# Kernel tuning notes

Measured on AMD Instinct MI355X. Metric: run time of the kernel, lower is better.

## Reference

```python
import jax, jax.numpy as jnp
import numpy as np

EMB = 1024
HEADS = 16


def setup_inputs() -> dict:
    key = jax.random.key(0)
    ks = jax.random.split(key, 5)
    s = 1.0 / np.sqrt(EMB).astype(np.float32)
    return {
        "x": jax.random.normal(ks[0], (4, 2048, EMB), dtype=jnp.float32),
        "Wq": jax.random.normal(ks[1], (EMB, EMB), dtype=jnp.float32) * s,
        "bq": jnp.zeros((EMB,), dtype=jnp.float32),
        "Wk": jax.random.normal(ks[2], (EMB, EMB), dtype=jnp.float32) * s,
        "bk": jnp.zeros((EMB,), dtype=jnp.float32),
        "Wv": jax.random.normal(ks[3], (EMB, EMB), dtype=jnp.float32) * s,
        "bv": jnp.zeros((EMB,), dtype=jnp.float32),
        "Wo": jax.random.normal(ks[4], (EMB, EMB), dtype=jnp.float32) * s,
        "bo": jnp.zeros((EMB,), dtype=jnp.float32),
    }


def reference(x, Wq, bq, Wk, bk, Wv, bv, Wo, bo):
    b, n, e = x.shape
    h = HEADS
    d = e // h
    # QKV projections, split heads: [b, n, e] -> [b, h, n, d]
    def split_heads(t):
        return t.reshape(b, n, h, d).transpose(0, 2, 1, 3)
    q = split_heads(x @ Wq + bq)
    k = split_heads(x @ Wk + bk)
    v = split_heads(x @ Wv + bv)
    # NOTE: original scales by sqrt(emb_size), not sqrt(head_dim)
    energy = jnp.einsum('bhqd,bhkd->bhqk', q, k)
    att = jax.nn.softmax(energy / jnp.sqrt(jnp.float32(e)), axis=-1)
    # dropout is identity in eval mode
    out = jnp.einsum('bhqk,bhkd->bhqd', att, v)
    out = out.transpose(0, 2, 1, 3).reshape(b, n, e)
    return out @ Wo + bo
```

## Files before the change

### kernel.cpp

```cpp
#include <hip/hip_runtime.h>

#define EMB   1024
#define SEQ   2048
#define BATCH 4
#define HEADS 16
#define HDIM  64
#define MTOT  8192

typedef __bf16 bf16x8 __attribute__((ext_vector_type(8)));
typedef float  fx4    __attribute__((ext_vector_type(4)));

#if __has_builtin(__builtin_amdgcn_exp2f)
#define EXP2(x) __builtin_amdgcn_exp2f(x)
#else
#define EXP2(x) exp2f(x)
#endif

__device__ __forceinline__ unsigned short f2bf(float f) {
    unsigned u = __builtin_bit_cast(unsigned, f);
    u += 0x7fffu + ((u >> 16) & 1u);
    return (unsigned short)(u >> 16);
}
__device__ __forceinline__ unsigned short bfbits(float f) {
    __bf16 h = (__bf16)f;
    return __builtin_bit_cast(unsigned short, h);
}

#define AS1 __attribute__((address_space(1)))
#define AS3 __attribute__((address_space(3)))
__device__ __forceinline__ void glds16(const void* g, void* l) {
    __builtin_amdgcn_global_load_lds((AS1 void*)g, (AS3 void*)l, 16, 0, 0);
}
#define DRAIN_GLDS() __builtin_amdgcn_s_waitcnt(0x0f70)

#define QSCALE 0.0450842137604569f

__global__ __launch_bounds__(256) void cvt_x_kernel(const float* __restrict__ x,
                                                    unsigned short* __restrict__ xb)
{
    const int idx = (blockIdx.x * 256 + threadIdx.x) * 4;
    const float4 v = *(const float4*)(x + idx);
    ushort4 o;
    o.x = f2bf(v.x); o.y = f2bf(v.y); o.z = f2bf(v.z); o.w = f2bf(v.w);
    *(ushort4*)(xb + idx) = o;
}

__global__ __launch_bounds__(256) void cvt_w_kernel(
    const float* __restrict__ w0, const float* __restrict__ w1,
    const float* __restrict__ w2, const float* __restrict__ w3,
    unsigned short* __restrict__ o0, unsigned short* __restrict__ o1,
    unsigned short* __restrict__ o2, unsigned short* __restrict__ o3)
{
    const int z = blockIdx.z;
    const float* W = z == 0 ? w0 : (z == 1 ? w1 : (z == 2 ? w2 : w3));
    unsigned short* O = z == 0 ? o0 : (z == 1 ? o1 : (z == 2 ? o2 : o3));

    __shared__ float Ws[64][65];
    const int t  = threadIdx.x;
    const int k0 = blockIdx.x * 64, n0 = blockIdx.y * 64;
#pragma unroll
    for (int p = 0; p < 4; ++p) {
        const int row = p * 16 + (t >> 4);
        const int col = (t & 15) * 4;
        const float4 v = *(const float4*)(W + (size_t)(k0 + row) * EMB + n0 + col);
        Ws[row][col]     = v.x; Ws[row][col + 1] = v.y;
        Ws[row][col + 2] = v.z; Ws[row][col + 3] = v.w;
    }
    __syncthreads();
    const int nn = t >> 2;
    const int kb = (t & 3) * 16;
#pragma unroll
    for (int q = 0; q < 2; ++q) {
        const int kk = kb + q * 8;
        ushort4 u0, u1;
        u0.x = f2bf(Ws[kk + 0][nn]); u0.y = f2bf(Ws[kk + 1][nn]);
        u0.z = f2bf(Ws[kk + 2][nn]); u0.w = f2bf(Ws[kk + 3][nn]);
        u1.x = f2bf(Ws[kk + 4][nn]); u1.y = f2bf(Ws[kk + 5][nn]);
        u1.z = f2bf(Ws[kk + 6][nn]); u1.w = f2bf(Ws[kk + 7][nn]);
        *(ushort4*)(O + (size_t)(n0 + nn) * EMB + k0 + kk)     = u0;
        *(ushort4*)(O + (size_t)(n0 + nn) * EMB + k0 + kk + 4) = u1;
    }
}

__global__ __launch_bounds__(256) void gemm_bf16_kernel(
    const unsigned short* __restrict__ Ag,
    const unsigned short* __restrict__ B0, const unsigned short* __restrict__ B1,
    const unsigned short* __restrict__ B2,
    const float* __restrict__ bias0, const float* __restrict__ bias1,
    const float* __restrict__ bias2,
    void* out0, void* out1, void* out2, int mode)
{
    const int z = blockIdx.z;
    const unsigned short* __restrict__ Bg = z == 0 ? B0 : (z == 1 ? B1 : B2);
    const float* __restrict__ bias = z == 0 ? bias0 : (z == 1 ? bias1 : bias2);
    void* outp = z == 0 ? out0 : (z == 1 ? out1 : out2);

    __shared__ unsigned short As[128][32];
    __shared__ unsigned short Bs[128][32];

    const int t    = threadIdx.x;
    const int w    = t >> 6;
    const int lane = t & 63;
    const int low4 = lane & 15;
    const int quad = lane >> 4;
    const int m0 = blockIdx.x * 128;
    const int e0 = blockIdx.y * 128;
    const int we = (w & 1) * 64;
    const int wm = (w >> 1) * 64;

    const int srow   = w * 32 + (lane >> 2);
    const int schunk = (lane & 3) ^ ((lane >> 3) & 3);
    const int scol   = schunk * 8;

    const int fchunk = (quad ^ ((low4 >> 1) & 3)) * 8;

    fx4 acc[4][4] = {};

    for (int k0 = 0; k0 < EMB; k0 += 32) {
        __syncthreads();
        glds16(Ag + (size_t)(m0 + srow) * EMB + k0 + scol,      &As[w * 32][0]);
        glds16(Ag + (size_t)(m0 + srow + 16) * EMB + k0 + scol, &As[w * 32 + 16][0]);
        glds16(Bg + (size_t)(e0 + srow) * EMB + k0 + scol,      &Bs[w * 32][0]);
        glds16(Bg + (size_t)(e0 + srow + 16) * EMB + k0 + scol, &Bs[w * 32 + 16][0]);
        DRAIN_GLDS();
        __syncthreads();

        bf16x8 af[4], bfr[4];
#pragma unroll
        for (int i = 0; i < 4; ++i) {
            af[i]  = *(const bf16x8*)&Bs[we + i * 16 + low4][fchunk];
            bfr[i] = *(const bf16x8*)&As[wm + i * 16 + low4][fchunk];
        }
#pragma unroll
        for (int i = 0; i < 4; ++i)
#pragma unroll
            for (int j = 0; j < 4; ++j)
                acc[i][j] = __builtin_amdgcn_mfma_f32_16x16x32_bf16(af[i], bfr[j], acc[i][j], 0, 0, 0);
    }

    fx4 bv[4];
#pragma unroll
    for (int i = 0; i < 4; ++i)
        bv[i] = *(const fx4*)(bias + e0 + we + i * 16 + quad * 4);

    if (mode == 1) {
#pragma unroll
        for (int i = 0; i < 4; ++i)
#pragma unroll
            for (int j = 0; j < 4; ++j) {
                const int m  = m0 + wm + j * 16 + low4;
                const int eb = e0 + we + i * 16 + quad * 4;
                fx4 o4;
#pragma unroll
                for (int rr = 0; rr < 4; ++rr) o4[rr] = acc[i][j][rr] + bv[i][rr];
                *(fx4*)((float*)outp + (size_t)m * EMB + eb) = o4;
            }
    } else if (z <= 1) {
        const float sc = (z == 0) ? QSCALE : 1.0f;
        unsigned short* o = (unsigned short*)outp;
#pragma unroll
        for (int i = 0; i < 4; ++i)
#pragma unroll
            for (int j = 0; j < 4; ++j) {
                const int m  = m0 + wm + j * 16 + low4;
                const int eb = e0 + we + i * 16 + quad * 4;
                const int bb = m >> 11, n = m & (SEQ - 1);
                const int hh = eb >> 6, db = eb & 63;
                ushort4 o4;
                o4.x = f2bf((acc[i][j][0] + bv[i][0]) * sc);
                o4.y = f2bf((acc[i][j][1] + bv[i][1]) * sc);
                o4.z = f2bf((acc[i][j][2] + bv[i][2]) * sc);
                o4.w = f2bf((acc[i][j][3] + bv[i][3]) * sc);
                *(ushort4*)(o + (((size_t)(bb * HEADS + hh)) * SEQ + n) * HDIM + db) = o4;
            }
    } else {
        unsigned short* o = (unsigned short*)outp;
        const int mbase = m0 + wm;
        const int bb    = mbase >> 11;
        const int nb    = mbase & (SEQ - 1);
#pragma unroll
        for (int i = 0; i < 4; ++i) {
            const int eb = e0 + we + i * 16 + quad * 4;
            const int hh = eb >> 6, db = eb & 63;
#pragma unroll
            for (int rr = 0; rr < 4; ++rr) {
                ushort4 o4;
                o4.x = f2bf(acc[i][0][rr] + bv[i][rr]);
                o4.y = f2bf(acc[i][1][rr] + bv[i][rr]);
                o4.z = f2bf(acc[i][2][rr] + bv[i][rr]);
                o4.w = f2bf(acc[i][3][rr] + bv[i][rr]);
                *(ushort4*)(o + (((size_t)(bb * HEADS + hh)) * HDIM + db + rr) * SEQ
                              + nb + low4 * 4) = o4;
            }
        }
    }
}

__global__ __launch_bounds__(256, 2) void attn_mfma5_kernel(
    const unsigned short* __restrict__ qg, const unsigned short* __restrict__ kg,
    const unsigned short* __restrict__ vg, unsigned short* __restrict__ attb)
{
    __shared__ unsigned short Ks[2][64][64];
    __shared__ unsigned short Vs[2][64][64];

    const int t    = threadIdx.x;
    const int w    = t >> 6;
    const int lane = t & 63;
    const int low4 = lane & 15;
    const int quad = lane >> 4;
    const int q0   = blockIdx.x * 256 + w * 64;
    const int bh   = blockIdx.y;
    const size_t base = (size_t)bh * SEQ * HDIM;

    const int srow8  = lane >> 3;
    const int schunk = (lane & 7) ^ srow8;

    const int tr  = 2 * (low4 >> 2) + (low4 & 1) + 8 * ((low4 >> 1) & 1);
    const int x7k = tr & 7;
    const int x7v = low4 & 7;

    bf16x8 aq[4][2];
#pragma unroll
    for (int s = 0; s < 4; ++s) {
        const size_t qrow = base + (size_t)(q0 + s * 16 + low4) * HDIM;
        aq[s][0] = *(const bf16x8*)(qg + qrow + quad * 8);
        aq[s][1] = *(const bf16x8*)(qg + qrow + 32 + quad * 8);
    }

    fx4 o_acc[4][4] = {};
    float l_part[4] = {};
    const fx4 fzero = {0.f, 0.f, 0.f, 0.f};

    {
        const unsigned short* kp = kg + base + (size_t)(w * 16 + srow8) * HDIM + schunk * 8;
        glds16(kp,              &Ks[0][w * 16][0]);
        glds16(kp + 8 * HDIM,   &Ks[0][w * 16 + 8][0]);
        const unsigned short* vp = vg + base + (size_t)(w * 16 + srow8) * SEQ + schunk * 8;
        glds16(vp,              &Vs[0][w * 16][0]);
        glds16(vp + 8 * SEQ,    &Vs[0][w * 16 + 8][0]);
    }

    for (int tt0 = 0; tt0 < SEQ / 64; ++tt0) {
        const int buf = tt0 & 1;
        DRAIN_GLDS();
        __syncthreads();

        bf16x8 kf[4][2], vf[4][2];
#pragma unroll
        for (int tk = 0; tk < 4; ++tk) {
#pragma unroll
            for (int c = 0; c < 2; ++c) {
                kf[tk][c] = *(const bf16x8*)&Ks[buf][tk * 16 + tr][(((c * 4 + quad) ^ x7k)) * 8];
                vf[tk][c] = *(const bf16x8*)&Vs[buf][tk * 16 + low4][(((c * 4 + quad) ^ x7v)) * 8];
            }
        }

        if (tt0 + 1 < SEQ / 64) {
            const int kv1 = (tt0 + 1) * 64;
            const unsigned short* kp = kg + base + (size_t)(kv1 + w * 16 + srow8) * HDIM + schunk * 8;
            glds16(kp,            &Ks[buf ^ 1][w * 16][0]);
            glds16(kp + 8 * HDIM, &Ks[buf ^ 1][w * 16 + 8][0]);
            const unsigned short* vp = vg + base + (size_t)(w * 16 + srow8) * SEQ + kv1 + schunk * 8;
            glds16(vp,            &Vs[buf ^ 1][w * 16][0]);
            glds16(vp + 8 * SEQ,  &Vs[buf ^ 1][w * 16 + 8][0]);
        }

#pragma unroll
        for (int s = 0; s < 4; ++s) {
            fx4 sa[4];
#pragma unroll
            for (int tk = 0; tk < 4; ++tk) {
                sa[tk] = __builtin_amdgcn_mfma_f32_16x16x32_bf16(kf[tk][0], aq[s][0], fzero, 0, 0, 0);
                sa[tk] = __builtin_amdgcn_mfma_f32_16x16x32_bf16(kf[tk][1], aq[s][1], sa[tk], 0, 0, 0);
            }
            float p[4][4];
#pragma unroll
            for (int tk = 0; tk < 4; ++tk)
#pragma unroll
                for (int r = 0; r < 4; ++r)
                    p[tk][r] = EXP2(sa[tk][r]);

            l_part[s] += (((p[0][0] + p[0][1]) + (p[0][2] + p[0][3]))
                        + ((p[1][0] + p[1][1]) + (p[1][2] + p[1][3])))
                       + (((p[2][0] + p[2][1]) + (p[2][2] + p[2][3]))
                        + ((p[3][0] + p[3][1]) + (p[3][2] + p[3][3])));

            bf16x8 pf0, pf1;
#pragma unroll
            for (int tk = 0; tk < 4; ++tk) {
                pf0[tk]     = (__bf16)p[tk][0];
                pf0[4 + tk] = (__bf16)p[tk][1];
                pf1[tk]     = (__bf16)p[tk][2];
                pf1[4 + tk] = (__bf16)p[tk][3];
            }
#pragma unroll
            for (int t2 = 0; t2 < 4; ++t2) {
                o_acc[s][t2] = __builtin_amdgcn_mfma_f32_16x16x32_bf16(vf[t2][0], pf0, o_acc[s][t2], 0, 0, 0);
                o_acc[s][t2] = __builtin_amdgcn_mfma_f32_16x16x32_bf16(vf[t2][1], pf1, o_acc[s][t2], 0, 0, 0);
            }
        }
    }

    float linv[4];
#pragma unroll
    for (int s = 0; s < 4; ++s) {
        float v = l_part[s];
        v += __shfl_xor(v, 16);
        v += __shfl_xor(v, 32);
        linv[s] = 1.0f / v;
    }

    const int bb = bh >> 4, hh = bh & 15;
#pragma unroll
    for (int s = 0; s < 4; ++s) {
        const size_t m = (size_t)bb * SEQ + q0 + s * 16 + low4;
#pragma unroll
        for (int t2 = 0; t2 < 4; ++t2) {
            ushort4 o4;
            o4.x = bfbits(o_acc[s][t2][0] * linv[s]);
            o4.y = bfbits(o_acc[s][t2][1] * linv[s]);
            o4.z = bfbits(o_acc[s][t2][2] * linv[s]);
            o4.w = bfbits(o_acc[s][t2][3] * linv[s]);
            *(ushort4*)(attb + m * EMB + hh * HDIM + t2 * 16 + quad * 4) = o4;
        }
    }
}

extern "C" void kernel_launch(void* const* d_in, const int* in_sizes, int n_in,
                              void* d_out, int out_size, void* d_ws, size_t ws_size,
                              hipStream_t stream)
{
    const float* x  = (const float*)d_in[0];
    const float* Wq = (const float*)d_in[1];
    const float* bq = (const float*)d_in[2];
    const float* Wk = (const float*)d_in[3];
    const float* bk = (const float*)d_in[4];
    const float* Wv = (const float*)d_in[5];
    const float* bv = (const float*)d_in[6];
    const float* Wo = (const float*)d_in[7];
    const float* bo = (const float*)d_in[8];

    unsigned short* ws  = (unsigned short*)d_ws;
    unsigned short* xb  = ws;
    unsigned short* wqt = xb + 8388608;
    unsigned short* wkt = wqt + 1048576;
    unsigned short* wvt = wkt + 1048576;
    unsigned short* wot = wvt + 1048576;
    unsigned short* qb  = wot + 1048576;
    unsigned short* kbuf = qb + 8388608;
    unsigned short* vtb  = kbuf + 8388608;
    unsigned short* attb = vtb + 8388608;

    cvt_x_kernel<<<8192, 256, 0, stream>>>(x, xb);
    cvt_w_kernel<<<dim3(16, 16, 4), 256, 0, stream>>>(Wq, Wk, Wv, Wo, wqt, wkt, wvt, wot);

    gemm_bf16_kernel<<<dim3(64, 8, 3), 256, 0, stream>>>(
        xb, wqt, wkt, wvt, bq, bk, bv, qb, kbuf, vtb, 0);

    attn_mfma5_kernel<<<dim3(8, 64), 256, 0, stream>>>(qb, kbuf, vtb, attb);

    gemm_bf16_kernel<<<dim3(64, 8, 1), 256, 0, stream>>>(
        attb, wot, wot, wot, bo, bo, bo, d_out, d_out, d_out, 1);
}
```

Measured before the change: 271.0 us.

## Replace QKV projection with 256x256-tile double-buffered fused GEMM kernel

Adds a dedicated QKV projection kernel that uses 256x256 output tiles, 512 threads, a 64-wide K step and double-buffered LDS staging through global_load_lds, with a swizzled block order for L2 locality. It treats Wq/Wk/Wv as one contiguous 3072-row weight matrix, which relies on their transposed copies being adjacent in the workspace. The goal is more data reuse per tile and overlap of loads with MFMA compared with the old 128x128 single-buffered GEMM. The cost is high register and LDS pressure (128 KB of LDS per block), which may limit occupancy.

```diff
diff --git a/kernel.cpp b/kernel.cpp
--- a/kernel.cpp
+++ b/kernel.cpp
@@ -32,6 +32,10 @@
     __builtin_amdgcn_global_load_lds((AS1 void*)g, (AS3 void*)l, 16, 0, 0);
 }
 #define DRAIN_GLDS() __builtin_amdgcn_s_waitcnt(0x0f70)
+
+#define BAR()    asm volatile("s_barrier" ::: "memory")
+#define WAITV8() asm volatile("s_waitcnt vmcnt(8)" ::: "memory")
+#define WAITV0() asm volatile("s_waitcnt vmcnt(0)" ::: "memory")
 
 #define QSCALE 0.0450842137604569f
 
@@ -82,6 +86,171 @@
     }
 }
 
+__device__ __forceinline__ void stage8(const unsigned short* xp, unsigned short* xd,
+                                       const unsigned short* wp, unsigned short* wd)
+{
+    glds16(xp,            xd);
+    glds16(xp +  8 * EMB, xd + 8 * 64);
+    glds16(xp + 16 * EMB, xd + 16 * 64);
+    glds16(xp + 24 * EMB, xd + 24 * 64);
+    glds16(wp,            wd);
+    glds16(wp +  8 * EMB, wd + 8 * 64);
+    glds16(wp + 16 * EMB, wd + 16 * 64);
+    glds16(wp + 24 * EMB, wd + 24 * 64);
+}
+
+__global__ __launch_bounds__(512, 2) void gemm_qkv256_kernel(
+    const unsigned short* __restrict__ Xg, const unsigned short* __restrict__ Wg,
+    const float* __restrict__ bq, const float* __restrict__ bk,
+    const float* __restrict__ bv,
+    unsigned short* __restrict__ qb, unsigned short* __restrict__ kb,
+    unsigned short* __restrict__ vtb)
+{
+    __shared__ unsigned short Xs[2][256][64];
+    __shared__ unsigned short Ws[2][256][64];
+
+    int lin = blockIdx.x;
+    lin = (lin & 7) * 48 + (lin >> 3);
+    const int bx  = lin & 31;
+    const int by  = lin >> 5;
+    const int m0  = bx * 256;
+    const int e0g = by * 256;
+
+    const int t    = threadIdx.x;
+    const int w    = t >> 6;
+    const int lane = t & 63;
+    const int low4 = lane & 15;
+    const int quad = lane >> 4;
+    const int wm   = w >> 2;
+    const int wn   = w & 3;
+
+    const int r8 = lane >> 3;
+    const int sc = (lane & 7) ^ r8;
+
+    const unsigned short* xrow = Xg + (size_t)(m0 + w * 32 + r8) * EMB + sc * 8;
+    const unsigned short* wrow = Wg + (size_t)(e0g + w * 32 + r8) * EMB + sc * 8;
+
+    fx4 acc[4][8] = {};
+
+    stage8(xrow,      &Xs[0][w * 32][0], wrow,      &Ws[0][w * 32][0]);
+    stage8(xrow + 64, &Xs[1][w * 32][0], wrow + 64, &Ws[1][w * 32][0]);
+    WAITV8();
+    BAR();
+
+#pragma unroll 2
+    for (int kt = 0; kt < 16; ++kt) {
+        unsigned short (*Xb)[64] = Xs[kt & 1];
+        unsigned short (*Wb)[64] = Ws[kt & 1];
+
+        {
+            bf16x8 wf[4], xf[8];
+#pragma unroll
+            for (int ni = 0; ni < 4; ++ni) {
+                const int row = wn * 64 + ni * 16 + low4;
+                wf[ni] = *(const bf16x8*)&Wb[row][((quad) ^ (row & 7)) * 8];
+            }
+#pragma unroll
+            for (int mi = 0; mi < 8; ++mi) {
+                const int row = wm * 128 + mi * 16 + low4;
+                xf[mi] = *(const bf16x8*)&Xb[row][((quad) ^ (row & 7)) * 8];
+            }
+            BAR();
+            __builtin_amdgcn_s_setprio(1);
+#pragma unroll
+            for (int ni = 0; ni < 4; ++ni)
+#pragma unroll
+                for (int mi = 0; mi < 8; ++mi)
+                    acc[ni][mi] = __builtin_amdgcn_mfma_f32_16x16x32_bf16(
+                        wf[ni], xf[mi], acc[ni][mi], 0, 0, 0);
+            __builtin_amdgcn_s_setprio(0);
+            BAR();
+        }
+        {
+            bf16x8 wf[4], xf[8];
+#pragma unroll
+            for (int ni = 0; ni < 4; ++ni) {
+                const int row = wn * 64 + ni * 16 + low4;
+                wf[ni] = *(const bf16x8*)&Wb[row][((4 + quad) ^ (row & 7)) * 8];
+            }
+#pragma unroll
+            for (int mi = 0; mi < 8; ++mi) {
+                const int row = wm * 128 + mi * 16 + low4;
+                xf[mi] = *(const bf16x8*)&Xb[row][((4 + quad) ^ (row & 7)) * 8];
+            }
+            BAR();
+            __builtin_amdgcn_s_setprio(1);
+#pragma unroll
+            for (int ni = 0; ni < 4; ++ni)
+#pragma unroll
+                for (int mi = 0; mi < 8; ++mi)
+                    acc[ni][mi] = __builtin_amdgcn_mfma_f32_16x16x32_bf16(
+                        wf[ni], xf[mi], acc[ni][mi], 0, 0, 0);
+            __builtin_amdgcn_s_setprio(0);
+            BAR();
+        }
+        if (kt + 2 < 16) {
+            stage8(xrow + (kt + 2) * 64, &Xb[w * 32][0],
+                   wrow + (kt + 2) * 64, &Wb[w * 32][0]);
+            WAITV8();
+            BAR();
+        } else if (kt + 1 < 16) {
+            WAITV0();
+            BAR();
+        }
+    }
+
+    const int z   = by >> 2;
+    const int eLb = (by & 3) * 256 + wn * 64;
+    const float* bias = z == 0 ? bq : (z == 1 ? bk : bv);
+    fx4 bvv[4];
+#pragma unroll
+    for (int ni = 0; ni < 4; ++ni)
+        bvv[ni] = *(const fx4*)(bias + eLb + ni * 16 + quad * 4);
+
+    if (z <= 1) {
+        const float scl = (z == 0) ? QSCALE : 1.0f;
+        unsigned short* o = (z == 0) ? qb : kb;
+#pragma unroll
+        for (int ni = 0; ni < 4; ++ni)
+#pragma unroll
+            for (int mi = 0; mi < 8; ++mi) {
+                const int m  = m0 + wm * 128 + mi * 16 + low4;
+                const int eL = eLb + ni * 16 + quad * 4;
+                const int bb = m >> 11, n = m & (SEQ - 1);
+                const int hh = eL >> 6, db = eL & 63;
+                ushort4 o4;
+                o4.x = f2bf((acc[ni][mi][0] + bvv[ni][0]) * scl);
+                o4.y = f2bf((acc[ni][mi][1] + bvv[ni][1]) * scl);
+                o4.z = f2bf((acc[ni][mi][2] + bvv[ni][2]) * scl);
+                o4.w = f2bf((acc[ni][mi][3] + bvv[ni][3]) * scl);
+                *(ushort4*)(o + (((size_t)(bb * HEADS + hh)) * SEQ + n) * HDIM + db) = o4;
+            }
+    } else {
+        unsigned short* o = vtb;
+#pragma unroll
+        for (int ni = 0; ni < 4; ++ni) {
+            const int eL = eLb + ni * 16 + quad * 4;
+            const int hh = eL >> 6, db = eL & 63;
+#pragma unroll
+            for (int g = 0; g < 2; ++g) {
+                const int mb = m0 + wm * 128 + g * 64;
+                const int bb = mb >> 11;
+                const int nb = mb & (SEQ - 1);
+#pragma unroll
+                for (int rr = 0; rr < 4; ++rr) {
+                    ushort4 o4;
+                    o4.x = f2bf(acc[ni][g * 4 + 0][rr] + bvv[ni][rr]);
+                    o4.y = f2bf(acc[ni][g * 4 + 1][rr] + bvv[ni][rr]);
+                    o4.z = f2bf(acc[ni][g * 4 + 2][rr] + bvv[ni][rr]);
+                    o4.w = f2bf(acc[ni][g * 4 + 3][rr] + bvv[ni][rr]);
+                    *(ushort4*)(o + (((size_t)(bb * HEADS + hh)) * HDIM + db + rr) * SEQ
+                                  + nb + low4 * 4) = o4;
+                }
+            }
+        }
+    }
+}
+
 __global__ __launch_bounds__(256) void gemm_bf16_kernel(
     const unsigned short* __restrict__ Ag,
     const unsigned short* __restrict__ B0, const unsigned short* __restrict__ B1,
@@ -111,7 +280,6 @@
     const int srow   = w * 32 + (lane >> 2);
     const int schunk = (lane & 3) ^ ((lane >> 3) & 3);
     const int scol   = schunk * 8;
-
     const int fchunk = (quad ^ ((low4 >> 1) & 3)) * 8;
 
     fx4 acc[4][4] = {};
@@ -354,8 +522,7 @@
     cvt_x_kernel<<<8192, 256, 0, stream>>>(x, xb);
     cvt_w_kernel<<<dim3(16, 16, 4), 256, 0, stream>>>(Wq, Wk, Wv, Wo, wqt, wkt, wvt, wot);
 
-    gemm_bf16_kernel<<<dim3(64, 8, 3), 256, 0, stream>>>(
-        xb, wqt, wkt, wvt, bq, bk, bv, qb, kbuf, vtb, 0);
+    gemm_qkv256_kernel<<<384, 512, 0, stream>>>(xb, wqt, bq, bk, bv, qb, kbuf, vtb);
 
     attn_mfma5_kernel<<<dim3(8, 64), 256, 0, stream>>>(qb, kbuf, vtb, attb);
 
```

Result: slower. 287.6 us (+6.1%).

## Double-buffer GEMM LDS tiles with BK=64 and overlap loads with MFMA

Applied to the files above, without the earlier changes.

The bf16 GEMM kernel now keeps two LDS buffers, each 64 elements deep in K with an 8-chunk XOR swizzle. It prefetches the next K tile via global_load_lds while running MFMAs on the current one, and uses one barrier per iteration instead of a full drain plus two barriers. Launch bounds add a minimum of 2 blocks per CU. The aim is to hide global load latency and halve loop and barrier overhead, at the cost of 64 KB of LDS per block, which may limit occupancy.

```diff
diff --git a/kernel.cpp b/kernel.cpp
--- a/kernel.cpp
+++ b/kernel.cpp
@@ -32,6 +32,9 @@
     __builtin_amdgcn_global_load_lds((AS1 void*)g, (AS3 void*)l, 16, 0, 0);
 }
 #define DRAIN_GLDS() __builtin_amdgcn_s_waitcnt(0x0f70)
+
+#define BAR()    asm volatile("s_barrier" ::: "memory")
+#define WAITV0() asm volatile("s_waitcnt vmcnt(0)" ::: "memory")
 
 #define QSCALE 0.0450842137604569f
 
@@ -82,7 +85,7 @@
     }
 }
 
-__global__ __launch_bounds__(256) void gemm_bf16_kernel(
+__global__ __launch_bounds__(256, 2) void gemm_bf16_kernel(
     const unsigned short* __restrict__ Ag,
     const unsigned short* __restrict__ B0, const unsigned short* __restrict__ B1,
     const unsigned short* __restrict__ B2,
@@ -95,8 +98,8 @@
     const float* __restrict__ bias = z == 0 ? bias0 : (z == 1 ? bias1 : bias2);
     void* outp = z == 0 ? out0 : (z == 1 ? out1 : out2);
 
-    __shared__ unsigned short As[128][32];
-    __shared__ unsigned short Bs[128][32];
+    __shared__ unsigned short As[2][128][64];
+    __shared__ unsigned short Bs[2][128][64];
 
     const int t    = threadIdx.x;
     const int w    = t >> 6;
@@ -108,34 +111,55 @@
     const int we = (w & 1) * 64;
     const int wm = (w >> 1) * 64;
 
-    const int srow   = w * 32 + (lane >> 2);
-    const int schunk = (lane & 3) ^ ((lane >> 3) & 3);
-    const int scol   = schunk * 8;
-
-    const int fchunk = (quad ^ ((low4 >> 1) & 3)) * 8;
+    const int srow8  = lane >> 3;
+    const int schunk = (lane & 7) ^ srow8;
+
+    const unsigned short* ap0 = Ag + (size_t)(m0 + w * 32 + srow8) * EMB + schunk * 8;
+    const unsigned short* bp0 = Bg + (size_t)(e0 + w * 32 + srow8) * EMB + schunk * 8;
+
+    auto stage = [&](int bf, int ko) {
+        const unsigned short* ap = ap0 + ko;
+        const unsigned short* bp = bp0 + ko;
+        glds16(ap,            &As[bf][w * 32 +  0][0]);
+        glds16(ap +  8 * EMB, &As[bf][w * 32 +  8][0]);
+        glds16(ap + 16 * EMB, &As[bf][w * 32 + 16][0]);
+        glds16(ap + 24 * EMB, &As[bf][w * 32 + 24][0]);
+        glds16(bp,            &Bs[bf][w * 32 +  0][0]);
+        glds16(bp +  8 * EMB, &Bs[bf][w * 32 +  8][0]);
+        glds16(bp + 16 * EMB, &Bs[bf][w * 32 + 16][0]);
+        glds16(bp + 24 * EMB, &Bs[bf][w * 32 + 24][0]);
+    };
 
     fx4 acc[4][4] = {};
 
-    for (int k0 = 0; k0 < EMB; k0 += 32) {
-        __syncthreads();
-        glds16(Ag + (size_t)(m0 + srow) * EMB + k0 + scol,      &As[w * 32][0]);
-        glds16(Ag + (size_t)(m0 + srow + 16) * EMB + k0 + scol, &As[w * 32 + 16][0]);
-        glds16(Bg + (size_t)(e0 + srow) * EMB + k0 + scol,      &Bs[w * 32][0]);
-        glds16(Bg + (size_t)(e0 + srow + 16) * EMB + k0 + scol, &Bs[w * 32 + 16][0]);
-        DRAIN_GLDS();
-        __syncthreads();
-
-        bf16x8 af[4], bfr[4];
-#pragma unroll
-        for (int i = 0; i < 4; ++i) {
-            af[i]  = *(const bf16x8*)&Bs[we + i * 16 + low4][fchunk];
-            bfr[i] = *(const bf16x8*)&As[wm + i * 16 + low4][fchunk];
-        }
-#pragma unroll
-        for (int i = 0; i < 4; ++i)
+    stage(0, 0);
+    WAITV0();
+    BAR();
+
+#pragma unroll 2
+    for (int kt = 0; kt < 16; ++kt) {
+        const int bf = kt & 1;
+        if (kt + 1 < 16) stage(bf ^ 1, (kt + 1) * 64);
+
+#pragma unroll
+        for (int ks = 0; ks < 2; ++ks) {
+            const int fch = ((ks * 4 + quad) ^ (low4 & 7)) * 8;
+            bf16x8 af[4], bfr[4];
+#pragma unroll
+            for (int i = 0; i < 4; ++i)
+                af[i] = *(const bf16x8*)&Bs[bf][we + i * 16 + low4][fch];
 #pragma unroll
             for (int j = 0; j < 4; ++j)
-                acc[i][j] = __builtin_amdgcn_mfma_f32_16x16x32_bf16(af[i], bfr[j], acc[i][j], 0, 0, 0);
+                bfr[j] = *(const bf16x8*)&As[bf][wm + j * 16 + low4][fch];
+#pragma unroll
+            for (int i = 0; i < 4; ++i)
+#pragma unroll
+                for (int j = 0; j < 4; ++j)
+                    acc[i][j] = __builtin_amdgcn_mfma_f32_16x16x32_bf16(af[i], bfr[j], acc[i][j], 0, 0, 0);
+        }
+
+        WAITV0();
+        BAR();
     }
 
     fx4 bv[4];
```

Result: no change. 267.6 us (-1.2%).
